# Kernel tuning notes

Measured on AMD Instinct MI355X. Metric: run time of the kernel, lower is better.

Reference implementation:

```python
import jax, jax.numpy as jnp
import numpy as np

MEMORY_SIZE = 40
INPUT_SIZE = 256
OUTPUT_SIZE = 256
BATCH = 16
SEQ = 4096


def setup_inputs() -> dict:
    key = jax.random.key(0)
    k1, k2, k3, k4 = jax.random.split(key, 4)
    x = jax.random.normal(k1, (BATCH, SEQ, INPUT_SIZE), dtype=jnp.float32)
    # xavier-uniform-style init for params
    lim_w = float(np.sqrt(6.0 / (INPUT_SIZE + OUTPUT_SIZE)))
    W1 = jax.random.uniform(k2, (INPUT_SIZE, OUTPUT_SIZE), minval=-lim_w, maxval=lim_w, dtype=jnp.float32)
    W2 = jax.random.uniform(k3, (INPUT_SIZE, OUTPUT_SIZE), minval=-lim_w, maxval=lim_w, dtype=jnp.float32)
    bias = jnp.ones((OUTPUT_SIZE,), dtype=jnp.float32)
    lim_m = float(np.sqrt(6.0 / (MEMORY_SIZE + 1 + INPUT_SIZE)))
    mw = jax.random.uniform(k4, (MEMORY_SIZE + 1, INPUT_SIZE), minval=-lim_m, maxval=lim_m, dtype=jnp.float32)
    mw = mw.at[0].set(0.0)  # torch init zeros row 0 (it stays trainable though)
    return {"input_data": x, "W1": W1, "W2": W2, "bias": bias, "memory_weights": mw}


def reference(input_data, W1, W2, bias, memory_weights):
    # Faithful to: idx(i,j) = i-j if 1 <= i-j <= memory_size else 0;
    # h_hatt[b,i,d] = sum_j memory_weights[idx(i,j), d] * x[b,j,d]
    # = sum_{l=1..m} w[l]*x[i-l]  +  w[0]*(sum_j x[j] - window sum).
    m = memory_weights.shape[0] - 1
    B, T, D = input_data.shape
    total = jnp.sum(input_data, axis=1, keepdims=True)  # [B,1,D]
    h_hatt = jnp.zeros_like(input_data)
    win = jnp.zeros_like(input_data)
    for l in range(1, m + 1):  # fixed small memory order
        shifted = jnp.pad(input_data[:, : T - l], ((0, 0), (l, 0), (0, 0)))
        h_hatt = h_hatt + memory_weights[l] * shifted
        win = win + shifted
    h_hatt = h_hatt + memory_weights[0] * (total - win)
    return input_data @ W1 + h_hatt @ W2 + bias
```

## Files before the change

### kernel.cpp

```cpp
#include <hip/hip_runtime.h>
#include <hip/hip_bf16.h>
#include <stdint.h>

#define NBATCH 16
#define SEQ 4096
#define DIM 256
#define MEM 40
#define KTOT 512
#define MTOT (NBATCH*SEQ)

typedef unsigned short u16;
typedef __attribute__((ext_vector_type(8))) short short8;
typedef __attribute__((ext_vector_type(4))) float f32x4;

typedef __attribute__((address_space(1))) const void gvoid_t;
typedef __attribute__((address_space(3))) void lvoid_t;

static __device__ __forceinline__ u16 f2bf(float f) {
    union { float f; uint32_t u; } v; v.f = f;
    uint32_t u = v.u;
    u += 0x7FFFu + ((u >> 16) & 1);
    return (u16)(u >> 16);
}

__global__ __launch_bounds__(256) void k_bmat(const float* __restrict__ W1,
                                              const float* __restrict__ W2,
                                              uint32_t* __restrict__ BmT32) {
    const int n = blockIdx.x;
    const int d = threadIdx.x;
    float w1 = W1[d * DIM + n];
    float w2 = W2[d * DIM + n];
    BmT32[n * DIM + d] = (uint32_t)f2bf(w1) | ((uint32_t)f2bf(w2) << 16);
}

#define TW 64

template <bool GUARD>
__device__ __forceinline__ void conv_wave(const float* __restrict__ xb,
                                          uint32_t* __restrict__ Ab,
                                          const float* __restrict__ mw,
                                          float* __restrict__ total,
                                          int d, int b, int t0, int g, bool lead) {
    const float mw0 = mw[d];
    float wt[20];
#pragma unroll
    for (int j = 0; j < 20; ++j)
        wt[j] = mw[(20 * g + j + 1) * DIM + d] - mw0;

    const int tg = t0 - 20 * g;
    float hist[20];
#pragma unroll
    for (int m = 0; m < 20; ++m) {
        int t = tg - 20 + m;
        if (GUARD)
            hist[m] = (t >= 0) ? xb[(size_t)t * DIM] : 0.0f;
        else
            hist[m] = xb[(size_t)t * DIM];
    }

    float colsum = 0.0f;
#pragma unroll
    for (int ch = 0; ch < TW / 4; ++ch) {
        const int tb = tg + ch * 4;
        float cur[4];
#pragma unroll
        for (int i = 0; i < 4; ++i) {
            int tt = tb + i;
            if (GUARD)
                cur[i] = (tt >= 0) ? xb[(size_t)tt * DIM] : 0.0f;
            else
                cur[i] = xb[(size_t)tt * DIM];
        }
        float h[4];
#pragma unroll
        for (int i = 0; i < 4; ++i) {
            float acc = 0.0f;
#pragma unroll
            for (int j = 0; j < 20; ++j) {
                int m = i + 19 - j;
                float v = (m < 20) ? hist[m] : cur[m - 20];
                acc = fmaf(wt[j], v, acc);
            }
            h[i] = acc;
        }
#pragma unroll
        for (int i = 0; i < 4; ++i) {
            float hs = h[i] + __shfl_xor(h[i], 32, 64);
            if (lead) {
                colsum += cur[i];
                __hip_bfloat162 p = __float22bfloat162_rn(make_float2(cur[i], hs));
                Ab[(size_t)(t0 + ch * 4 + i) * DIM] = *reinterpret_cast<uint32_t*>(&p);
            }
        }
#pragma unroll
        for (int m = 0; m < 16; ++m) hist[m] = hist[m + 4];
#pragma unroll
        for (int i = 0; i < 4; ++i) hist[16 + i] = cur[i];
    }
    if (lead) atomicAdd(&total[b * DIM + d], colsum);
}

__global__ void k_conv(const float* __restrict__ x,
                       const float* __restrict__ mw,
                       uint32_t* __restrict__ Aout,
                       float* __restrict__ total) {
    const int tid  = threadIdx.x;
    const int lane = tid & 63;
    const int w    = tid >> 6;
    const int c    = lane & 31;
    const int g    = lane >> 5;
    const int d    = blockIdx.z * 128 + w * 32 + c;
    const int b    = blockIdx.y;
    const int t0   = blockIdx.x * TW;

    const float* xb = x + (size_t)b * SEQ * DIM + d;
    uint32_t* Ab    = Aout + (size_t)b * SEQ * DIM + d;

    if (blockIdx.x == 0)
        conv_wave<true >(xb, Ab, mw, total, d, b, t0, g, g == 0);
    else
        conv_wave<false>(xb, Ab, mw, total, d, b, t0, g, g == 0);
}

__global__ __launch_bounds__(256) void k_corr(const float* __restrict__ W2,
                                              const float* __restrict__ bias,
                                              const float* __restrict__ mw,
                                              const float* __restrict__ total,
                                              float* __restrict__ corr) {
    const int b = blockIdx.x;
    const int n = threadIdx.x;
    float s = bias[n];
    for (int dd = 0; dd < DIM; ++dd)
        s += mw[dd] * total[b * DIM + dd] * W2[dd * DIM + n];
    corr[b * DIM + n] = s;
}

#define BM 128
#define BN 256
#define BK 64

__global__ __launch_bounds__(512) void k_gemm(const u16* A,
                                              const u16* __restrict__ BmT,
                                              const float* __restrict__ corr,
                                              float* out) {
    __shared__ __align__(16) u16 Alds[BM * BK];
    __shared__ __align__(16) u16 Blds[BN * BK];

    const int tid  = threadIdx.x;
    const int lane = tid & 63;
    const int w    = tid >> 6;
    const int wr   = w >> 2;
    const int wc   = w & 3;
    const int bid  = blockIdx.x;
    const int swz  = (bid & 7) * 64 + (bid >> 3);
    const int m0   = swz * BM;

    f32x4 acc[4][4] = {};

    for (int kt = 0; kt < KTOT / BK; ++kt) {
        const int k0 = kt * BK;
#pragma unroll
        for (int i = 0; i < 2; ++i) {
            int c   = i * 512 + tid;
            int row = c >> 3;
            int kin = (c & 7) * 8;
            const u16* g = A + ((size_t)(m0 + row) * KTOT + k0 + kin);
            char* l = (char*)Alds + (size_t)(i * 512 + (tid & ~63)) * 16;
            __builtin_amdgcn_global_load_lds((gvoid_t*)g, (lvoid_t*)l, 16, 0, 0);
        }
#pragma unroll
        for (int i = 0; i < 4; ++i) {
            int c   = i * 512 + tid;
            int n   = c >> 3;
            int kin = (c & 7) * 8;
            const u16* g = BmT + ((size_t)n * KTOT + k0 + kin);
            char* l = (char*)Blds + (size_t)(i * 512 + (tid & ~63)) * 16;
            __builtin_amdgcn_global_load_lds((gvoid_t*)g, (lvoid_t*)l, 16, 0, 0);
        }
        __syncthreads();

#pragma unroll
        for (int kk = 0; kk < 2; ++kk) {
            short8 af[4], bfr[4];
#pragma unroll
            for (int mi = 0; mi < 4; ++mi) {
                int r = wr * 64 + mi * 16 + (lane & 15);
                af[mi] = *(const short8*)(Alds + r * BK + kk * 32 + ((lane >> 4) * 8));
            }
#pragma unroll
            for (int ni = 0; ni < 4; ++ni) {
                int ccol = wc * 64 + ni * 16 + (lane & 15);
                bfr[ni] = *(const short8*)(Blds + ccol * BK + kk * 32 + ((lane >> 4) * 8));
            }
#pragma unroll
            for (int mi = 0; mi < 4; ++mi)
#pragma unroll
                for (int ni = 0; ni < 4; ++ni)
                    acc[mi][ni] = __builtin_amdgcn_mfma_f32_16x16x32_bf16(
                        af[mi], bfr[ni], acc[mi][ni], 0, 0, 0);
        }
        __syncthreads();
    }

    const int bidx = m0 >> 12;
    const float* corr_b = corr + bidx * DIM;
#pragma unroll
    for (int ni = 0; ni < 4; ++ni) {
        int col = wc * 64 + ni * 16 + (lane & 15);
        float cv = corr_b[col];
#pragma unroll
        for (int mi = 0; mi < 4; ++mi) {
            int rbase = m0 + wr * 64 + mi * 16 + ((lane >> 4) * 4);
#pragma unroll
            for (int j = 0; j < 4; ++j)
                out[(size_t)(rbase + j) * DIM + col] = acc[mi][ni][j] + cv;
        }
    }
}

extern "C" void kernel_launch(void* const* d_in, const int* in_sizes, int n_in,
                              void* d_out, int out_size, void* d_ws, size_t ws_size,
                              hipStream_t stream) {
    const float* x    = (const float*)d_in[0];
    const float* W1   = (const float*)d_in[1];
    const float* W2   = (const float*)d_in[2];
    const float* bias = (const float*)d_in[3];
    const float* mw   = (const float*)d_in[4];
    float* out = (float*)d_out;

    u16*   BmT   = (u16*)d_ws;
    float* total = (float*)((char*)d_ws + 262144);
    float* corr  = (float*)((char*)d_ws + 262144 + 16384);

    hipMemsetAsync(total, 0, NBATCH * DIM * sizeof(float), stream);
    k_bmat<<<dim3(DIM), dim3(256), 0, stream>>>(W1, W2, (uint32_t*)BmT);
    k_conv<<<dim3(SEQ / TW, NBATCH, 2), dim3(256), 0, stream>>>(
        x, mw, (uint32_t*)d_out, total);
    k_corr<<<dim3(NBATCH), dim3(256), 0, stream>>>(W2, bias, mw, total, corr);
    k_gemm<<<dim3(MTOT / BM), dim3(512), 0, stream>>>(
        (const u16*)d_out, BmT, corr, out);
}
```

Measured before the change: 94.45 us.

## Split conv taps four ways across lanes and vectorize columns as float2

```diff
diff --git a/kernel.cpp b/kernel.cpp
--- a/kernel.cpp
+++ b/kernel.cpp
@@ -36,68 +36,80 @@
 #define TW 64
 
 template <bool GUARD>
-__device__ __forceinline__ void conv_wave(const float* __restrict__ xb,
-                                          uint32_t* __restrict__ Ab,
-                                          const float* __restrict__ mw,
+__device__ __forceinline__ void conv_wave(const float2* __restrict__ xb,
+                                          uint2* __restrict__ Ab,
+                                          const float2* __restrict__ mwp,
                                           float* __restrict__ total,
-                                          int d, int b, int t0, int g, bool lead) {
-    const float mw0 = mw[d];
-    float wt[20];
-#pragma unroll
-    for (int j = 0; j < 20; ++j)
-        wt[j] = mw[(20 * g + j + 1) * DIM + d] - mw0;
-
-    const int tg = t0 - 20 * g;
-    float hist[20];
-#pragma unroll
-    for (int m = 0; m < 20; ++m) {
-        int t = tg - 20 + m;
-        if (GUARD)
-            hist[m] = (t >= 0) ? xb[(size_t)t * DIM] : 0.0f;
-        else
-            hist[m] = xb[(size_t)t * DIM];
-    }
-
-    float colsum = 0.0f;
+                                          int dpair, int b, int t0, int g, bool lead) {
+    const int LD = DIM / 2;
+    const float2 mw0 = mwp[0];
+    float2 wt[10];
+#pragma unroll
+    for (int j = 0; j < 10; ++j) {
+        float2 m = mwp[(size_t)(10 * g + 1 + j) * LD];
+        wt[j] = make_float2(m.x - mw0.x, m.y - mw0.y);
+    }
+
+    const int tg = t0 - 10 * g;
+    float2 hist[10];
+#pragma unroll
+    for (int m = 0; m < 10; ++m) {
+        int t = tg - 10 + m;
+        if (GUARD) hist[m] = (t >= 0) ? xb[(size_t)t * LD] : make_float2(0.f, 0.f);
+        else       hist[m] = xb[(size_t)t * LD];
+    }
+
+    float2 colsum = make_float2(0.f, 0.f);
 #pragma unroll
     for (int ch = 0; ch < TW / 4; ++ch) {
-        const int tb = tg + ch * 4;
-        float cur[4];
-#pragma unroll
-        for (int i = 0; i < 4; ++i) {
-            int tt = tb + i;
-            if (GUARD)
-                cur[i] = (tt >= 0) ? xb[(size_t)tt * DIM] : 0.0f;
-            else
-                cur[i] = xb[(size_t)tt * DIM];
-        }
-        float h[4];
-#pragma unroll
-        for (int i = 0; i < 4; ++i) {
-            float acc = 0.0f;
-#pragma unroll
-            for (int j = 0; j < 20; ++j) {
-                int m = i + 19 - j;
-                float v = (m < 20) ? hist[m] : cur[m - 20];
-                acc = fmaf(wt[j], v, acc);
-            }
-            h[i] = acc;
-        }
-#pragma unroll
-        for (int i = 0; i < 4; ++i) {
-            float hs = h[i] + __shfl_xor(h[i], 32, 64);
+        float2 cur[4];
+#pragma unroll
+        for (int i = 0; i < 4; ++i) {
+            int tt = tg + ch * 4 + i;
+            if (GUARD) cur[i] = (tt >= 0) ? xb[(size_t)tt * LD] : make_float2(0.f, 0.f);
+            else       cur[i] = xb[(size_t)tt * LD];
+        }
+        float2 h[4];
+#pragma unroll
+        for (int i = 0; i < 4; ++i) {
+            float ax0 = 0.f, ay0 = 0.f, ax1 = 0.f, ay1 = 0.f;
+#pragma unroll
+            for (int j = 0; j < 10; ++j) {
+                int m = i + 9 - j;
+                float2 v = (m < 10) ? hist[m] : cur[m - 10];
+                if (j & 1) { ax1 = fmaf(wt[j].x, v.x, ax1); ay1 = fmaf(wt[j].y, v.y, ay1); }
+                else       { ax0 = fmaf(wt[j].x, v.x, ax0); ay0 = fmaf(wt[j].y, v.y, ay0); }
+            }
+            h[i] = make_float2(ax0 + ax1, ay0 + ay1);
+        }
+#pragma unroll
+        for (int i = 0; i < 4; ++i) {
+            float hx = h[i].x;
+            hx += __shfl_xor(hx, 16, 64);
+            hx += __shfl_xor(hx, 32, 64);
+            float hy = h[i].y;
+            hy += __shfl_xor(hy, 16, 64);
+            hy += __shfl_xor(hy, 32, 64);
             if (lead) {
-                colsum += cur[i];
-                __hip_bfloat162 p = __float22bfloat162_rn(make_float2(cur[i], hs));
-                Ab[(size_t)(t0 + ch * 4 + i) * DIM] = *reinterpret_cast<uint32_t*>(&p);
-            }
-        }
-#pragma unroll
-        for (int m = 0; m < 16; ++m) hist[m] = hist[m + 4];
-#pragma unroll
-        for (int i = 0; i < 4; ++i) hist[16 + i] = cur[i];
-    }
-    if (lead) atomicAdd(&total[b * DIM + d], colsum);
+                colsum.x += cur[i].x;
+                colsum.y += cur[i].y;
+                __hip_bfloat162 p0 = __float22bfloat162_rn(make_float2(cur[i].x, hx));
+                __hip_bfloat162 p1 = __float22bfloat162_rn(make_float2(cur[i].y, hy));
+                uint2 st;
+                st.x = *reinterpret_cast<uint32_t*>(&p0);
+                st.y = *reinterpret_cast<uint32_t*>(&p1);
+                Ab[(size_t)(t0 + ch * 4 + i) * LD] = st;
+            }
+        }
+#pragma unroll
+        for (int m = 0; m < 6; ++m) hist[m] = hist[m + 4];
+#pragma unroll
+        for (int m = 6; m < 10; ++m) hist[m] = cur[m - 6];
+    }
+    if (lead) {
+        atomicAdd(&total[b * DIM + dpair], colsum.x);
+        atomicAdd(&total[b * DIM + dpair + 1], colsum.y);
+    }
 }
 
 __global__ void k_conv(const float* __restrict__ x,
@@ -107,19 +119,20 @@
     const int tid  = threadIdx.x;
     const int lane = tid & 63;
     const int w    = tid >> 6;
-    const int c    = lane & 31;
-    const int g    = lane >> 5;
-    const int d    = blockIdx.z * 128 + w * 32 + c;
+    const int c2   = lane & 15;
+    const int g    = lane >> 4;
     const int b    = blockIdx.y;
     const int t0   = blockIdx.x * TW;
-
-    const float* xb = x + (size_t)b * SEQ * DIM + d;
-    uint32_t* Ab    = Aout + (size_t)b * SEQ * DIM + d;
+    const int dpair = blockIdx.z * 128 + w * 32 + c2 * 2;
+
+    const float2* xb  = (const float2*)(x + (size_t)b * SEQ * DIM + dpair);
+    uint2* Ab         = (uint2*)(Aout + (size_t)b * SEQ * DIM + dpair);
+    const float2* mwp = (const float2*)(mw + dpair);
 
     if (blockIdx.x == 0)
-        conv_wave<true >(xb, Ab, mw, total, d, b, t0, g, g == 0);
+        conv_wave<true >(xb, Ab, mwp, total, dpair, b, t0, g, g == 0);
     else
-        conv_wave<false>(xb, Ab, mw, total, d, b, t0, g, g == 0);
+        conv_wave<false>(xb, Ab, mwp, total, dpair, b, t0, g, g == 0);
 }
 
 __global__ __launch_bounds__(256) void k_corr(const float* __restrict__ W2,
```

Result: slower. 109.0 us (+15.4%).
